# Performance work log

Hardware: AMD Instinct MI355X
Metric: run time of the kernel (lower is better)

## Reference

```python
import jax, jax.numpy as jnp
import numpy as np

N, D, C = 1_000_000, 50, 256


def setup_inputs() -> dict:
    key = jax.random.key(0)
    kx, kp = jax.random.split(key)
    X = jax.random.normal(kx, (N, D), dtype=jnp.float32)
    Phi = jax.random.normal(kp, (C, D), dtype=jnp.float32)  # learned centroid table new_Phi
    return {"X": X, "Phi": Phi}


def reference(X, Phi):
    # torch.cdist(X, Phi) then argmin(dim=1).
    # argmin over Euclidean distance == argmin over squared distance, so we
    x2 = jnp.sum(X * X, axis=-1, keepdims=True)          # [N, 1]
    p2 = jnp.sum(Phi * Phi, axis=-1)                      # [C]
    d2 = x2 + p2 - 2.0 * jnp.matmul(X, Phi.T)             # [N, C]
    y_pred = jnp.argmin(d2, axis=1).astype(jnp.int32)     # [N]
    return y_pred
```

## Files before the change

### kernel.cpp

```cpp
#include <hip/hip_runtime.h>
#include <math.h>

#define NPTS 1000000
#define DIM 50
#define NC 256
#define TAU 0.05f
#define MR 2
#define NTILES (NPTS / (MR * 16))

typedef short bf16x8 __attribute__((ext_vector_type(8)));
typedef float f32x4 __attribute__((ext_vector_type(4)));

__device__ __forceinline__ short f2bf(float f) {
    unsigned u = __builtin_bit_cast(unsigned, f);
    unsigned r = (u + 0x7FFFu + ((u >> 16) & 1u)) >> 16;
    return (short)r;
}
__device__ __forceinline__ float bf2f(short h) {
    unsigned u = ((unsigned)(unsigned short)h) << 16;
    return __builtin_bit_cast(float, u);
}
__device__ __forceinline__ void cvt8(const float* v, bf16x8& hi, bf16x8& lo) {
#pragma unroll
    for (int j = 0; j < 8; ++j) {
        short h = f2bf(v[j]);
        hi[j] = h;
        lo[j] = f2bf(v[j] - bf2f(h));
    }
}

__global__ void __launch_bounds__(256) prep_kernel(const float* __restrict__ Phi,
                                                   short* __restrict__ frag,
                                                   float* __restrict__ p2) {
    int tid = threadIdx.x;
    {
        const float* p = Phi + tid * DIM;
        float s = 0.f;
#pragma unroll
        for (int d = 0; d < DIM; ++d) s = fmaf(p[d], p[d], s);
        p2[tid] = s;
    }
    for (int it = tid; it < 4096; it += 256) {
        int lane = it & 63;
        int rest = it >> 6;
        int split = rest & 1;
        int ks = (rest >> 1) & 1;
        int ct = rest >> 2;
        int col = lane & 15;
        int kb = ks * 32 + ((lane >> 4) << 3);
        const float* pr = Phi + (ct * 16 + col) * DIM;
        short* dst = frag + (size_t)it * 8;
#pragma unroll
        for (int j = 0; j < 8; ++j) {
            int k = kb + j;
            float v = (k < DIM) ? pr[k] : 0.f;
            short h = f2bf(v);
            dst[j] = (split == 0) ? h : f2bf(v - bf2f(h));
        }
    }
}

__device__ void exact_row(const float* __restrict__ X, const float* __restrict__ Phi,
                          const float* __restrict__ p2, int* __restrict__ out, int row) {
    int lane = threadIdx.x & 63;
    const float* xr = X + (size_t)row * DIM;
    float x2 = 0.f;
#pragma unroll
    for (int d = 0; d < DIM; ++d) x2 = fmaf(xr[d], xr[d], x2);
    float best = INFINITY;
    int bi = 0;
    for (int i = 0; i < 4; ++i) {
        int c = lane * 4 + i;
        const float* pr = Phi + c * DIM;
        float a = 0.f;
#pragma unroll
        for (int d = 0; d < DIM; ++d) a = fmaf(xr[d], pr[d], a);
        float sc = (x2 + p2[c]) - 2.0f * a;
        if (sc < best) { best = sc; bi = c; }
    }
#pragma unroll
    for (int m = 1; m < 64; m <<= 1) {
        float ob = __shfl_xor(best, m);
        int oi = __shfl_xor(bi, m);
        if (ob < best || (ob == best && oi < bi)) { best = ob; bi = oi; }
    }
    if (lane == 0) out[row] = bi;
}

__global__ void __launch_bounds__(512, 4) assign_kernel(const float* __restrict__ X,
                                                        const float* __restrict__ Phi,
                                                        const int4* __restrict__ BfI,
                                                        const float* __restrict__ p2,
                                                        int* __restrict__ out) {
    __shared__ int4 Bs[4096];

#pragma unroll
    for (int j = 0; j < 8; ++j)
        Bs[threadIdx.x + j * 512] = BfI[threadIdx.x + j * 512];
    __syncthreads();

    int lane = threadIdx.x & 63;
    int wid = threadIdx.x >> 6;
    int t = blockIdx.x * 8 + wid;
    if (t >= NTILES) return;
    int tbase = t * (MR * 16);
    int colRow = lane & 15;
    int kgrp = lane >> 4;

    const bf16x8* Bsf = (const bf16x8*)Bs;

    bf16x8 Ahi[MR][2], Alo[MR][2];
#pragma unroll
    for (int mr = 0; mr < MR; ++mr) {
        const float* xp = X + (size_t)(tbase + mr * 16 + colRow) * DIM;
        {
            float v[8];
            const float2* q = (const float2*)(xp + (kgrp << 3));
#pragma unroll
            for (int h = 0; h < 4; ++h) { float2 e = q[h]; v[2 * h] = e.x; v[2 * h + 1] = e.y; }
            cvt8(v, Ahi[mr][0], Alo[mr][0]);
        }
        {
            float v[8];
#pragma unroll
            for (int h = 0; h < 4; ++h) {
                int o = 32 + (kgrp << 3) + 2 * h;
                int oc = (o <= 48) ? o : 48;
                float2 e = *(const float2*)(xp + oc);
                bool valid = (o <= 48);
                v[2 * h]     = valid ? e.x : 0.f;
                v[2 * h + 1] = valid ? e.y : 0.f;
            }
            cvt8(v, Ahi[mr][1], Alo[mr][1]);
        }
    }

    float best[MR][4], sec[MR][4];
    int bidx[MR][4];
#pragma unroll
    for (int mr = 0; mr < MR; ++mr)
#pragma unroll
        for (int r = 0; r < 4; ++r) { best[mr][r] = INFINITY; sec[mr][r] = INFINITY; bidx[mr][r] = 0; }

#pragma unroll 2
    for (int ct = 0; ct < 16; ++ct) {
        bf16x8 b0h = Bsf[((ct * 2 + 0) * 2 + 0) * 64 + lane];
        bf16x8 b0l = Bsf[((ct * 2 + 0) * 2 + 1) * 64 + lane];
        bf16x8 b1h = Bsf[((ct * 2 + 1) * 2 + 0) * 64 + lane];
        bf16x8 b1l = Bsf[((ct * 2 + 1) * 2 + 1) * 64 + lane];
        float p2v = p2[ct * 16 + colRow];
        int idx = ct * 16 + colRow;
#pragma unroll
        for (int mr = 0; mr < MR; ++mr) {
            f32x4 acc = {0.f, 0.f, 0.f, 0.f};
            acc = __builtin_amdgcn_mfma_f32_16x16x32_bf16(Alo[mr][0], b0h, acc, 0, 0, 0);
            acc = __builtin_amdgcn_mfma_f32_16x16x32_bf16(Ahi[mr][0], b0l, acc, 0, 0, 0);
            acc = __builtin_amdgcn_mfma_f32_16x16x32_bf16(Ahi[mr][0], b0h, acc, 0, 0, 0);
            acc = __builtin_amdgcn_mfma_f32_16x16x32_bf16(Alo[mr][1], b1h, acc, 0, 0, 0);
            acc = __builtin_amdgcn_mfma_f32_16x16x32_bf16(Ahi[mr][1], b1l, acc, 0, 0, 0);
            acc = __builtin_amdgcn_mfma_f32_16x16x32_bf16(Ahi[mr][1], b1h, acc, 0, 0, 0);
#pragma unroll
            for (int r = 0; r < 4; ++r) {
                float sc = fmaf(-2.0f, acc[r], p2v);
                if (sc < best[mr][r]) { sec[mr][r] = best[mr][r]; best[mr][r] = sc; bidx[mr][r] = idx; }
                else if (sc < sec[mr][r]) { sec[mr][r] = sc; }
            }
        }
    }

#pragma unroll
    for (int mr = 0; mr < MR; ++mr) {
#pragma unroll
        for (int r = 0; r < 4; ++r) {
            float b = best[mr][r], s = sec[mr][r];
            int bi = bidx[mr][r];
#pragma unroll
            for (int m = 1; m <= 8; m <<= 1) {
                float ob = __shfl_xor(b, m);
                float os = __shfl_xor(s, m);
                int oi = __shfl_xor(bi, m);
                float ns = fminf(fmaxf(b, ob), fminf(s, os));
                if (ob < b || (ob == b && oi < bi)) { b = ob; bi = oi; }
                s = ns;
            }
            bool flag = (s - b) < TAU;
            if ((lane & 15) == 0 && !flag)
                out[tbase + mr * 16 + (lane >> 4) * 4 + r] = bi;
            unsigned long long mb = __ballot(flag) & 0x0001000100010001ULL;
            while (mb) {
                int g = __builtin_ctzll(mb) >> 4;
                mb &= mb - 1;
                exact_row(X, Phi, p2, out, tbase + mr * 16 + g * 4 + r);
            }
        }
    }
}

extern "C" void kernel_launch(void* const* d_in, const int* in_sizes, int n_in,
                              void* d_out, int out_size, void* d_ws, size_t ws_size,
                              hipStream_t stream) {
    const float* X   = (const float*)d_in[0];
    const float* Phi = (const float*)d_in[1];
    int* out = (int*)d_out;
    short* frag = (short*)d_ws;
    float* p2   = (float*)((char*)d_ws + 65536);

    prep_kernel<<<1, 256, 0, stream>>>(Phi, frag, p2);
    int nblk = (NTILES + 7) / 8;
    assign_kernel<<<nblk, 512, 0, stream>>>(X, Phi, (const int4*)frag, p2, out);
}
```

Before: 439.0 us.

## Halve LDS with two-phase centroid staging and pack argmin index into score bits

After: 836.9 us. 90.6% more time.

```diff
diff --git a/kernel.cpp b/kernel.cpp
--- a/kernel.cpp
+++ b/kernel.cpp
@@ -31,7 +31,8 @@
 
 __global__ void __launch_bounds__(256) prep_kernel(const float* __restrict__ Phi,
                                                    short* __restrict__ frag,
-                                                   float* __restrict__ p2) {
+                                                   float* __restrict__ p2,
+                                                   float* __restrict__ p2b) {
     int tid = threadIdx.x;
     {
         const float* p = Phi + tid * DIM;
@@ -39,6 +40,7 @@
 #pragma unroll
         for (int d = 0; d < DIM; ++d) s = fmaf(p[d], p[d], s);
         p2[tid] = s;
+        p2b[tid] = 256.0f + s;
     }
     for (int it = tid; it < 4096; it += 256) {
         int lane = it & 63;
@@ -87,110 +89,128 @@
     if (lane == 0) out[row] = bi;
 }
 
-__global__ void __launch_bounds__(512, 4) assign_kernel(const float* __restrict__ X,
+__global__ void __launch_bounds__(512, 8) assign_kernel(const float* __restrict__ X,
                                                         const float* __restrict__ Phi,
                                                         const int4* __restrict__ BfI,
                                                         const float* __restrict__ p2,
+                                                        const float* __restrict__ p2b,
                                                         int* __restrict__ out) {
-    __shared__ int4 Bs[4096];
-
-#pragma unroll
-    for (int j = 0; j < 8; ++j)
-        Bs[threadIdx.x + j * 512] = BfI[threadIdx.x + j * 512];
-    __syncthreads();
-
-    int lane = threadIdx.x & 63;
-    int wid = threadIdx.x >> 6;
+    __shared__ int4 Bs[2048];
+    __shared__ float P2s[256];
+
+    int tid = threadIdx.x;
+    int lane = tid & 63;
+    int wid = tid >> 6;
     int t = blockIdx.x * 8 + wid;
-    if (t >= NTILES) return;
+    bool active = (t < NTILES);
     int tbase = t * (MR * 16);
     int colRow = lane & 15;
     int kgrp = lane >> 4;
-
     const bf16x8* Bsf = (const bf16x8*)Bs;
 
+#pragma unroll
+    for (int j = 0; j < 4; ++j)
+        Bs[tid + j * 512] = BfI[tid + j * 512];
+    if (tid < 256) P2s[tid] = p2b[tid];
+
     bf16x8 Ahi[MR][2], Alo[MR][2];
-#pragma unroll
-    for (int mr = 0; mr < MR; ++mr) {
-        const float* xp = X + (size_t)(tbase + mr * 16 + colRow) * DIM;
-        {
-            float v[8];
-            const float2* q = (const float2*)(xp + (kgrp << 3));
-#pragma unroll
-            for (int h = 0; h < 4; ++h) { float2 e = q[h]; v[2 * h] = e.x; v[2 * h + 1] = e.y; }
-            cvt8(v, Ahi[mr][0], Alo[mr][0]);
-        }
-        {
-            float v[8];
-#pragma unroll
-            for (int h = 0; h < 4; ++h) {
-                int o = 32 + (kgrp << 3) + 2 * h;
-                int oc = (o <= 48) ? o : 48;
-                float2 e = *(const float2*)(xp + oc);
-                bool valid = (o <= 48);
-                v[2 * h]     = valid ? e.x : 0.f;
-                v[2 * h + 1] = valid ? e.y : 0.f;
-            }
-            cvt8(v, Ahi[mr][1], Alo[mr][1]);
-        }
-    }
-
-    float best[MR][4], sec[MR][4];
-    int bidx[MR][4];
-#pragma unroll
-    for (int mr = 0; mr < MR; ++mr)
-#pragma unroll
-        for (int r = 0; r < 4; ++r) { best[mr][r] = INFINITY; sec[mr][r] = INFINITY; bidx[mr][r] = 0; }
-
+    unsigned pm1[MR][4], pm2[MR][4];
+    if (active) {
+#pragma unroll
+        for (int mr = 0; mr < MR; ++mr) {
+            const float* xp = X + (size_t)(tbase + mr * 16 + colRow) * DIM;
+            {
+                float v[8];
+                const float2* q = (const float2*)(xp + (kgrp << 3));
+#pragma unroll
+                for (int h = 0; h < 4; ++h) { float2 e = q[h]; v[2 * h] = e.x; v[2 * h + 1] = e.y; }
+                cvt8(v, Ahi[mr][0], Alo[mr][0]);
+            }
+            {
+                float v[8];
+#pragma unroll
+                for (int h = 0; h < 4; ++h) {
+                    int o = 32 + (kgrp << 3) + 2 * h;
+                    int oc = (o <= 48) ? o : 48;
+                    float2 e = *(const float2*)(xp + oc);
+                    bool valid = (o <= 48);
+                    v[2 * h]     = valid ? e.x : 0.f;
+                    v[2 * h + 1] = valid ? e.y : 0.f;
+                }
+                cvt8(v, Ahi[mr][1], Alo[mr][1]);
+            }
+        }
+#pragma unroll
+        for (int mr = 0; mr < MR; ++mr)
+#pragma unroll
+            for (int r = 0; r < 4; ++r) { pm1[mr][r] = 0xFFFFFFFFu; pm2[mr][r] = 0xFFFFFFFFu; }
+    }
+
+    auto process8 = [&](int phase) {
 #pragma unroll 2
-    for (int ct = 0; ct < 16; ++ct) {
-        bf16x8 b0h = Bsf[((ct * 2 + 0) * 2 + 0) * 64 + lane];
-        bf16x8 b0l = Bsf[((ct * 2 + 0) * 2 + 1) * 64 + lane];
-        bf16x8 b1h = Bsf[((ct * 2 + 1) * 2 + 0) * 64 + lane];
-        bf16x8 b1l = Bsf[((ct * 2 + 1) * 2 + 1) * 64 + lane];
-        float p2v = p2[ct * 16 + colRow];
-        int idx = ct * 16 + colRow;
+        for (int c8 = 0; c8 < 8; ++c8) {
+            int ct = phase * 8 + c8;
+            bf16x8 b0h = Bsf[(c8 * 4 + 0) * 64 + lane];
+            bf16x8 b0l = Bsf[(c8 * 4 + 1) * 64 + lane];
+            bf16x8 b1h = Bsf[(c8 * 4 + 2) * 64 + lane];
+            bf16x8 b1l = Bsf[(c8 * 4 + 3) * 64 + lane];
+            float p2v = P2s[ct * 16 + colRow];
+            unsigned vidx = (unsigned)(ct * 16 + colRow);
+#pragma unroll
+            for (int mr = 0; mr < MR; ++mr) {
+                f32x4 acc = {0.f, 0.f, 0.f, 0.f};
+                acc = __builtin_amdgcn_mfma_f32_16x16x32_bf16(Alo[mr][0], b0h, acc, 0, 0, 0);
+                acc = __builtin_amdgcn_mfma_f32_16x16x32_bf16(Ahi[mr][0], b0l, acc, 0, 0, 0);
+                acc = __builtin_amdgcn_mfma_f32_16x16x32_bf16(Ahi[mr][0], b0h, acc, 0, 0, 0);
+                acc = __builtin_amdgcn_mfma_f32_16x16x32_bf16(Alo[mr][1], b1h, acc, 0, 0, 0);
+                acc = __builtin_amdgcn_mfma_f32_16x16x32_bf16(Ahi[mr][1], b1l, acc, 0, 0, 0);
+                acc = __builtin_amdgcn_mfma_f32_16x16x32_bf16(Ahi[mr][1], b1h, acc, 0, 0, 0);
+#pragma unroll
+                for (int r = 0; r < 4; ++r) {
+                    float sc = fmaf(-2.0f, acc[r], p2v);
+                    unsigned u = (__builtin_bit_cast(unsigned, sc) & ~255u) | vidx;
+                    unsigned u2 = max(pm1[mr][r], u);
+                    pm2[mr][r] = min(pm2[mr][r], u2);
+                    pm1[mr][r] = min(pm1[mr][r], u);
+                }
+            }
+        }
+    };
+
+    __syncthreads();
+    if (active) process8(0);
+    __syncthreads();
+#pragma unroll
+    for (int j = 0; j < 4; ++j)
+        Bs[tid + j * 512] = BfI[2048 + tid + j * 512];
+    __syncthreads();
+    if (active) process8(1);
+
+    if (active) {
 #pragma unroll
         for (int mr = 0; mr < MR; ++mr) {
-            f32x4 acc = {0.f, 0.f, 0.f, 0.f};
-            acc = __builtin_amdgcn_mfma_f32_16x16x32_bf16(Alo[mr][0], b0h, acc, 0, 0, 0);
-            acc = __builtin_amdgcn_mfma_f32_16x16x32_bf16(Ahi[mr][0], b0l, acc, 0, 0, 0);
-            acc = __builtin_amdgcn_mfma_f32_16x16x32_bf16(Ahi[mr][0], b0h, acc, 0, 0, 0);
-            acc = __builtin_amdgcn_mfma_f32_16x16x32_bf16(Alo[mr][1], b1h, acc, 0, 0, 0);
-            acc = __builtin_amdgcn_mfma_f32_16x16x32_bf16(Ahi[mr][1], b1l, acc, 0, 0, 0);
-            acc = __builtin_amdgcn_mfma_f32_16x16x32_bf16(Ahi[mr][1], b1h, acc, 0, 0, 0);
 #pragma unroll
             for (int r = 0; r < 4; ++r) {
-                float sc = fmaf(-2.0f, acc[r], p2v);
-                if (sc < best[mr][r]) { sec[mr][r] = best[mr][r]; best[mr][r] = sc; bidx[mr][r] = idx; }
-                else if (sc < sec[mr][r]) { sec[mr][r] = sc; }
-            }
-        }
-    }
-
-#pragma unroll
-    for (int mr = 0; mr < MR; ++mr) {
-#pragma unroll
-        for (int r = 0; r < 4; ++r) {
-            float b = best[mr][r], s = sec[mr][r];
-            int bi = bidx[mr][r];
-#pragma unroll
-            for (int m = 1; m <= 8; m <<= 1) {
-                float ob = __shfl_xor(b, m);
-                float os = __shfl_xor(s, m);
-                int oi = __shfl_xor(bi, m);
-                float ns = fminf(fmaxf(b, ob), fminf(s, os));
-                if (ob < b || (ob == b && oi < bi)) { b = ob; bi = oi; }
-                s = ns;
-            }
-            bool flag = (s - b) < TAU;
-            if ((lane & 15) == 0 && !flag)
-                out[tbase + mr * 16 + (lane >> 4) * 4 + r] = bi;
-            unsigned long long mb = __ballot(flag) & 0x0001000100010001ULL;
-            while (mb) {
-                int g = __builtin_ctzll(mb) >> 4;
-                mb &= mb - 1;
-                exact_row(X, Phi, p2, out, tbase + mr * 16 + g * 4 + r);
+                unsigned a1 = pm1[mr][r], a2 = pm2[mr][r];
+#pragma unroll
+                for (int m = 1; m <= 8; m <<= 1) {
+                    unsigned b1 = (unsigned)__shfl_xor((int)a1, m);
+                    unsigned b2 = (unsigned)__shfl_xor((int)a2, m);
+                    a2 = min(min(a2, b2), max(a1, b1));
+                    a1 = min(a1, b1);
+                }
+                float f1 = __builtin_bit_cast(float, a1 & ~255u);
+                float f2 = __builtin_bit_cast(float, a2 & ~255u);
+                bool flag = (f2 - f1) < TAU;
+                int bi = (int)(a1 & 255u);
+                if ((lane & 15) == 0 && !flag)
+                    out[tbase + mr * 16 + (lane >> 4) * 4 + r] = bi;
+                unsigned long long mb = __ballot(flag) & 0x0001000100010001ULL;
+                while (mb) {
+                    int g = __builtin_ctzll(mb) >> 4;
+                    mb &= mb - 1;
+                    exact_row(X, Phi, p2, out, tbase + mr * 16 + g * 4 + r);
+                }
             }
         }
     }
@@ -201,11 +221,12 @@
                               hipStream_t stream) {
     const float* X   = (const float*)d_in[0];
     const float* Phi = (const float*)d_in[1];
-    int* out = (int*)d_out;
+    int* out   = (int*)d_out;
     short* frag = (short*)d_ws;
     float* p2   = (float*)((char*)d_ws + 65536);
-
-    prep_kernel<<<1, 256, 0, stream>>>(Phi, frag, p2);
+    float* p2b  = (float*)((char*)d_ws + 65536 + 1024);
+
+    prep_kernel<<<1, 256, 0, stream>>>(Phi, frag, p2, p2b);
     int nblk = (NTILES + 7) / 8;
-    assign_kernel<<<nblk, 512, 0, stream>>>(X, Phi, (const int4*)frag, p2, out);
-}
+    assign_kernel<<<nblk, 512, 0, stream>>>(X, Phi, (const int4*)frag, p2, p2b, out);
+}
```
